# Kernel tuning notes

Hardware: AMD Instinct MI355X
Metric: run time of the kernel (lower is better)

Reference implementation:

```python
import jax, jax.numpy as jnp
import numpy as np

N_NODES = 100000
N_EDGES = 1600000
D_FEAT = 64
K = 8
AVG_DEGREE = 16


def setup_inputs() -> dict:
    key = jax.random.key(0)
    k1, k2, k3, k4 = jax.random.split(key, 4)
    x = jax.random.normal(k1, (N_NODES, D_FEAT), dtype=jnp.float32)
    # scale weights ~1/degree so repeated propagation stays bounded
    edge_weight = jax.random.uniform(k2, (N_EDGES,), dtype=jnp.float32) / AVG_DEGREE
    src = jax.random.randint(k3, (N_EDGES,), 0, N_NODES)
    dst = jax.random.randint(k4, (N_EDGES,), 0, N_NODES)
    return {"x": x, "edge_weight": edge_weight, "src": src, "dst": dst}


def reference(x, edge_weight, src, dst):
    # Prop.forward: x = spmm(adj, x) repeated K times; returned value is adj^K @ x.
    # (The in-place y.add_(x) accumulator mutates the input tensor but is not returned.)
    n = x.shape[0]
    w = edge_weight[:, None]  # [E,1]

    def step(h, _):
        # one spmm: out[dst] += w * h[src]
        h = jax.ops.segment_sum(w * h[src], dst, num_segments=n)
        return h, None

    x, _ = jax.lax.scan(step, x, None, length=K)
    return x
```

## Files before the change

### kernel.cpp

```cpp
#include <hip/hip_runtime.h>

#define N_NODES 100000
#define N_EDGES 1600000
#define D_FEAT  64
#define K_STEPS 8
#define NB_SCAN ((N_NODES + 255) / 256)

typedef unsigned long long u64;
typedef float f4 __attribute__((ext_vector_type(4)));

__global__ void k_zero(int* __restrict__ p, int n) {
    int i = blockIdx.x * blockDim.x + threadIdx.x;
    if (i < n) p[i] = 0;
}

__global__ void k_hist(const int* __restrict__ dst, int* __restrict__ counts,
                       int* __restrict__ rank, int n) {
    int i = blockIdx.x * blockDim.x + threadIdx.x;
    if (i < n) rank[i] = atomicAdd(&counts[dst[i]], 1);
}

__global__ void k_bsum(const int* __restrict__ counts, int* __restrict__ blockSums, int n) {
    __shared__ int ws[4];
    int t = threadIdx.x;
    int i = blockIdx.x * 256 + t;
    int c = (i < n) ? counts[i] : 0;
    for (int off = 32; off; off >>= 1) c += __shfl_down(c, off);
    if ((t & 63) == 0) ws[t >> 6] = c;
    __syncthreads();
    if (t == 0) blockSums[blockIdx.x] = ws[0] + ws[1] + ws[2] + ws[3];
}

__global__ void k_sscan(const int* __restrict__ blockSums, int* __restrict__ blockPrefix,
                        int* __restrict__ offsets, int nb, int n) {
    __shared__ int sh[512];
    int t = threadIdx.x;
    int v = (t < nb) ? blockSums[t] : 0;
    sh[t] = v;
    __syncthreads();
    for (int off = 1; off < 512; off <<= 1) {
        int u = (t >= off) ? sh[t - off] : 0;
        __syncthreads();
        sh[t] += u;
        __syncthreads();
    }
    if (t < nb) blockPrefix[t] = sh[t] - v;
    if (t == 511) offsets[n] = sh[511];
}

__global__ void k_bscan(const int* __restrict__ counts, const int* __restrict__ blockPrefix,
                        int* __restrict__ offsets, int n) {
    __shared__ int sh[256];
    int t = threadIdx.x;
    int i = blockIdx.x * 256 + t;
    int c = (i < n) ? counts[i] : 0;
    sh[t] = c;
    __syncthreads();
    for (int off = 1; off < 256; off <<= 1) {
        int u = (t >= off) ? sh[t - off] : 0;
        __syncthreads();
        sh[t] += u;
        __syncthreads();
    }
    int excl = sh[t] - c + blockPrefix[blockIdx.x];
    if (i < n) offsets[i] = excl;
}

__global__ void k_scatter(const int* __restrict__ src, const int* __restrict__ dst,
                          const float* __restrict__ w, const int* __restrict__ offsets,
                          const int* __restrict__ rank, u64* __restrict__ csr, int n) {
    int i = blockIdx.x * blockDim.x + threadIdx.x;
    if (i < n) {
        int d = dst[i];
        int pos = offsets[d] + rank[i];
        u64 p = ((u64)__float_as_uint(w[i]) << 32) | (unsigned)src[i];
        __builtin_nontemporal_store(p, &csr[pos]);
    }
}

__global__ void k_prop(const float* __restrict__ hin, float* __restrict__ hout,
                       const int* __restrict__ offsets,
                       const u64* __restrict__ csr, int n) {
    int wave = (blockIdx.x * blockDim.x + threadIdx.x) >> 6;
    int lane = threadIdx.x & 63;
    if (wave >= n) return;
    int b = offsets[wave];
    int e = offsets[wave + 1];
    int eg = lane >> 3;
    int fl = lane & 7;
    f4 a0 = {0.f, 0.f, 0.f, 0.f};
    f4 a1 = {0.f, 0.f, 0.f, 0.f};
    for (int i = b + eg; i < e; i += 8) {
        u64 p   = __builtin_nontemporal_load(&csr[i]);
        int s   = (int)(p & 0xffffffffu);
        float w = __uint_as_float((unsigned)(p >> 32));
        const f4* row = reinterpret_cast<const f4*>(&hin[((size_t)s << 6) + (fl << 3)]);
        f4 v0 = row[0];
        f4 v1 = row[1];
        a0.x = fmaf(w, v0.x, a0.x);
        a0.y = fmaf(w, v0.y, a0.y);
        a0.z = fmaf(w, v0.z, a0.z);
        a0.w = fmaf(w, v0.w, a0.w);
        a1.x = fmaf(w, v1.x, a1.x);
        a1.y = fmaf(w, v1.y, a1.y);
        a1.z = fmaf(w, v1.z, a1.z);
        a1.w = fmaf(w, v1.w, a1.w);
    }
    #pragma unroll
    for (int off = 8; off < 64; off <<= 1) {
        a0.x += __shfl_xor(a0.x, off);
        a0.y += __shfl_xor(a0.y, off);
        a0.z += __shfl_xor(a0.z, off);
        a0.w += __shfl_xor(a0.w, off);
        a1.x += __shfl_xor(a1.x, off);
        a1.y += __shfl_xor(a1.y, off);
        a1.z += __shfl_xor(a1.z, off);
        a1.w += __shfl_xor(a1.w, off);
    }
    if (eg == 0) {
        f4* o = reinterpret_cast<f4*>(&hout[((size_t)wave << 6) + (fl << 3)]);
        __builtin_nontemporal_store(a0, &o[0]);
        __builtin_nontemporal_store(a1, &o[1]);
    }
}

extern "C" void kernel_launch(void* const* d_in, const int* in_sizes, int n_in,
                              void* d_out, int out_size, void* d_ws, size_t ws_size,
                              hipStream_t stream) {
    const float* x   = (const float*)d_in[0];
    const float* ew  = (const float*)d_in[1];
    const int*   src = (const int*)d_in[2];
    const int*   dst = (const int*)d_in[3];
    float* out = (float*)d_out;

    float* hA         = (float*)d_ws;
    int*   rank       = (int*)d_ws;
    u64*   csr        = (u64*)(hA + (size_t)N_NODES * D_FEAT);
    int*   offsets    = (int*)(csr + N_EDGES);
    int*   counts     = offsets + (N_NODES + 1);
    int*   blockSums  = counts + N_NODES;
    int*   blockPref  = blockSums + NB_SCAN;

    k_zero<<<(N_NODES + 255) / 256, 256, 0, stream>>>(counts, N_NODES);
    k_hist<<<(N_EDGES + 255) / 256, 256, 0, stream>>>(dst, counts, rank, N_EDGES);
    k_bsum<<<NB_SCAN, 256, 0, stream>>>(counts, blockSums, N_NODES);
    k_sscan<<<1, 512, 0, stream>>>(blockSums, blockPref, offsets, NB_SCAN, N_NODES);
    k_bscan<<<NB_SCAN, 256, 0, stream>>>(counts, blockPref, offsets, N_NODES);
    k_scatter<<<(N_EDGES + 255) / 256, 256, 0, stream>>>(src, dst, ew, offsets, rank,
                                                         csr, N_EDGES);

    const int prop_grid = (N_NODES * 64 + 255) / 256;
    const float* in = x;
    for (int k = 0; k < K_STEPS; ++k) {
        float* o = ((k & 1) == 0) ? hA : out;
        k_prop<<<prop_grid, 256, 0, stream>>>(in, o, offsets, csr, N_NODES);
        in = o;
    }
}
```

Baseline: 615.8 us.

## Sort CSR edges within each destination by source tile, use cached output stores

The CSR build now groups each destination's edges by source-index tile (16 tiles). It does this with a per-tile histogram, a per-node tile prefix scan, and tile-aware scatter positions. The aim is more locality and coherence in the gathers of hin rows during propagation. The output stores in k_prop also switch from nontemporal to normal stores, so the next step's reads may hit in cache. In exchange, preprocessing gets larger: a 16x counts array, an extra kernel, and more atomic spread.

```diff
diff --git a/kernel.cpp b/kernel.cpp
--- a/kernel.cpp
+++ b/kernel.cpp
@@ -5,19 +5,40 @@
 #define D_FEAT  64
 #define K_STEPS 8
 #define NB_SCAN ((N_NODES + 255) / 256)
+#define TILES   16
+#define TILE_W  6250
 
 typedef unsigned long long u64;
 typedef float f4 __attribute__((ext_vector_type(4)));
+
+__device__ __forceinline__ int src_tile(int s) { return (int)((unsigned)s / (unsigned)TILE_W); }
 
 __global__ void k_zero(int* __restrict__ p, int n) {
     int i = blockIdx.x * blockDim.x + threadIdx.x;
     if (i < n) p[i] = 0;
 }
 
-__global__ void k_hist(const int* __restrict__ dst, int* __restrict__ counts,
-                       int* __restrict__ rank, int n) {
+__global__ void k_hist(const int* __restrict__ dst, const int* __restrict__ src,
+                       int* __restrict__ cnt16, int* __restrict__ rank, int n) {
     int i = blockIdx.x * blockDim.x + threadIdx.x;
-    if (i < n) rank[i] = atomicAdd(&counts[dst[i]], 1);
+    if (i < n) {
+        int t = src_tile(src[i]);
+        rank[i] = atomicAdd(&cnt16[t * N_NODES + dst[i]], 1);
+    }
+}
+
+__global__ void k_tilescan(const int* __restrict__ cnt16, int* __restrict__ tilePre,
+                           int* __restrict__ counts, int n) {
+    int v = blockIdx.x * blockDim.x + threadIdx.x;
+    if (v >= n) return;
+    int run = 0;
+    #pragma unroll
+    for (int t = 0; t < TILES; ++t) {
+        int c = cnt16[t * N_NODES + v];
+        tilePre[t * N_NODES + v] = run;
+        run += c;
+    }
+    counts[v] = run;
 }
 
 __global__ void k_bsum(const int* __restrict__ counts, int* __restrict__ blockSums, int n) {
@@ -68,12 +89,15 @@
 
 __global__ void k_scatter(const int* __restrict__ src, const int* __restrict__ dst,
                           const float* __restrict__ w, const int* __restrict__ offsets,
-                          const int* __restrict__ rank, u64* __restrict__ csr, int n) {
+                          const int* __restrict__ tilePre, const int* __restrict__ rank,
+                          u64* __restrict__ csr, int n) {
     int i = blockIdx.x * blockDim.x + threadIdx.x;
     if (i < n) {
+        int s = src[i];
         int d = dst[i];
-        int pos = offsets[d] + rank[i];
-        u64 p = ((u64)__float_as_uint(w[i]) << 32) | (unsigned)src[i];
+        int t = src_tile(s);
+        int pos = offsets[d] + tilePre[t * N_NODES + d] + rank[i];
+        u64 p = ((u64)__float_as_uint(w[i]) << 32) | (unsigned)s;
         __builtin_nontemporal_store(p, &csr[pos]);
     }
 }
@@ -119,8 +143,8 @@
     }
     if (eg == 0) {
         f4* o = reinterpret_cast<f4*>(&hout[((size_t)wave << 6) + (fl << 3)]);
-        __builtin_nontemporal_store(a0, &o[0]);
-        __builtin_nontemporal_store(a1, &o[1]);
+        o[0] = a0;
+        o[1] = a1;
     }
 }
 
@@ -135,19 +159,22 @@
 
     float* hA         = (float*)d_ws;
     int*   rank       = (int*)d_ws;
+    int*   cnt16      = rank + N_EDGES;
+    int*   tilePre    = cnt16 + TILES * N_NODES;
     u64*   csr        = (u64*)(hA + (size_t)N_NODES * D_FEAT);
     int*   offsets    = (int*)(csr + N_EDGES);
     int*   counts     = offsets + (N_NODES + 1);
     int*   blockSums  = counts + N_NODES;
     int*   blockPref  = blockSums + NB_SCAN;
 
-    k_zero<<<(N_NODES + 255) / 256, 256, 0, stream>>>(counts, N_NODES);
-    k_hist<<<(N_EDGES + 255) / 256, 256, 0, stream>>>(dst, counts, rank, N_EDGES);
+    k_zero<<<(TILES * N_NODES + 255) / 256, 256, 0, stream>>>(cnt16, TILES * N_NODES);
+    k_hist<<<(N_EDGES + 255) / 256, 256, 0, stream>>>(dst, src, cnt16, rank, N_EDGES);
+    k_tilescan<<<(N_NODES + 255) / 256, 256, 0, stream>>>(cnt16, tilePre, counts, N_NODES);
     k_bsum<<<NB_SCAN, 256, 0, stream>>>(counts, blockSums, N_NODES);
     k_sscan<<<1, 512, 0, stream>>>(blockSums, blockPref, offsets, NB_SCAN, N_NODES);
     k_bscan<<<NB_SCAN, 256, 0, stream>>>(counts, blockPref, offsets, N_NODES);
-    k_scatter<<<(N_EDGES + 255) / 256, 256, 0, stream>>>(src, dst, ew, offsets, rank,
-                                                         csr, N_EDGES);
+    k_scatter<<<(N_EDGES + 255) / 256, 256, 0, stream>>>(src, dst, ew, offsets, tilePre,
+                                                         rank, csr, N_EDGES);
 
     const int prop_grid = (N_NODES * 64 + 255) / 256;
     const float* in = x;
```

After: 612.4 us. No clear change (-0.6%).

## Split features into eight sliced layouts and propagate per slice

Applied to the files above, without the earlier changes.

Reshapes the node feature matrix into eight 8-feature slices, each stored contiguously, so every propagation block gathers one slice. One wave now handles one node for a single slice, with one scalar FMA per lane. Added reshape and unshape kernels convert the layout before and after the eight steps. The intent is a smaller gather working set per slice, but block indexing interleaves slices, so all slices are still touched concurrently. It also re-reads each node's CSR edge list once per slice, eight times per step, and launches eight times as many waves with less work each.

```diff
diff --git a/kernel.cpp b/kernel.cpp
--- a/kernel.cpp
+++ b/kernel.cpp
@@ -5,9 +5,11 @@
 #define D_FEAT  64
 #define K_STEPS 8
 #define NB_SCAN ((N_NODES + 255) / 256)
+#define SLICE_F 8
+#define SLICES  8
+#define SLICE_ELEMS ((size_t)N_NODES * SLICE_F)
 
 typedef unsigned long long u64;
-typedef float f4 __attribute__((ext_vector_type(4)));
 
 __global__ void k_zero(int* __restrict__ p, int n) {
     int i = blockIdx.x * blockDim.x + threadIdx.x;
@@ -78,50 +80,47 @@
     }
 }
 
-__global__ void k_prop(const float* __restrict__ hin, float* __restrict__ hout,
-                       const int* __restrict__ offsets,
-                       const u64* __restrict__ csr, int n) {
-    int wave = (blockIdx.x * blockDim.x + threadIdx.x) >> 6;
-    int lane = threadIdx.x & 63;
-    if (wave >= n) return;
-    int b = offsets[wave];
-    int e = offsets[wave + 1];
+__global__ void k_reshape(const float* __restrict__ x, float* __restrict__ hsl, int total) {
+    int tid = blockIdx.x * blockDim.x + threadIdx.x;
+    if (tid >= total) return;
+    int f = tid & 7;
+    int v = (tid >> 3) % N_NODES;
+    int s = tid / (N_NODES * 8);
+    hsl[tid] = x[(size_t)v * D_FEAT + s * 8 + f];
+}
+
+__global__ void k_unshape(const float* __restrict__ hsl, float* __restrict__ out, int total) {
+    int tid = blockIdx.x * blockDim.x + threadIdx.x;
+    if (tid >= total) return;
+    int j = tid & 63;
+    int v = tid >> 6;
+    out[tid] = hsl[(size_t)(j >> 3) * SLICE_ELEMS + (size_t)v * SLICE_F + (j & 7)];
+}
+
+__global__ __launch_bounds__(256)
+void k_prop_slice(const float* __restrict__ hin, float* __restrict__ hout,
+                  const int* __restrict__ offsets, const u64* __restrict__ csr, int n) {
+    int slice = blockIdx.x & 7;
+    int node  = (blockIdx.x >> 3) * 4 + (threadIdx.x >> 6);
+    int lane  = threadIdx.x & 63;
+    if (node >= n) return;
+    int b = offsets[node];
+    int e = offsets[node + 1];
     int eg = lane >> 3;
     int fl = lane & 7;
-    f4 a0 = {0.f, 0.f, 0.f, 0.f};
-    f4 a1 = {0.f, 0.f, 0.f, 0.f};
+    const float* hs = hin + (size_t)slice * SLICE_ELEMS;
+    float acc = 0.f;
     for (int i = b + eg; i < e; i += 8) {
         u64 p   = __builtin_nontemporal_load(&csr[i]);
         int s   = (int)(p & 0xffffffffu);
         float w = __uint_as_float((unsigned)(p >> 32));
-        const f4* row = reinterpret_cast<const f4*>(&hin[((size_t)s << 6) + (fl << 3)]);
-        f4 v0 = row[0];
-        f4 v1 = row[1];
-        a0.x = fmaf(w, v0.x, a0.x);
-        a0.y = fmaf(w, v0.y, a0.y);
-        a0.z = fmaf(w, v0.z, a0.z);
-        a0.w = fmaf(w, v0.w, a0.w);
-        a1.x = fmaf(w, v1.x, a1.x);
-        a1.y = fmaf(w, v1.y, a1.y);
-        a1.z = fmaf(w, v1.z, a1.z);
-        a1.w = fmaf(w, v1.w, a1.w);
+        acc = fmaf(w, hs[s * SLICE_F + fl], acc);
     }
-    #pragma unroll
-    for (int off = 8; off < 64; off <<= 1) {
-        a0.x += __shfl_xor(a0.x, off);
-        a0.y += __shfl_xor(a0.y, off);
-        a0.z += __shfl_xor(a0.z, off);
-        a0.w += __shfl_xor(a0.w, off);
-        a1.x += __shfl_xor(a1.x, off);
-        a1.y += __shfl_xor(a1.y, off);
-        a1.z += __shfl_xor(a1.z, off);
-        a1.w += __shfl_xor(a1.w, off);
-    }
-    if (eg == 0) {
-        f4* o = reinterpret_cast<f4*>(&hout[((size_t)wave << 6) + (fl << 3)]);
-        __builtin_nontemporal_store(a0, &o[0]);
-        __builtin_nontemporal_store(a1, &o[1]);
-    }
+    acc += __shfl_xor(acc, 8);
+    acc += __shfl_xor(acc, 16);
+    acc += __shfl_xor(acc, 32);
+    if (eg == 0)
+        hout[(size_t)slice * SLICE_ELEMS + (size_t)node * SLICE_F + fl] = acc;
 }
 
 extern "C" void kernel_launch(void* const* d_in, const int* in_sizes, int n_in,
@@ -133,13 +132,15 @@
     const int*   dst = (const int*)d_in[3];
     float* out = (float*)d_out;
 
-    float* hA         = (float*)d_ws;
+    float* hS0        = (float*)d_ws;
     int*   rank       = (int*)d_ws;
-    u64*   csr        = (u64*)(hA + (size_t)N_NODES * D_FEAT);
+    u64*   csr        = (u64*)(hS0 + (size_t)N_NODES * D_FEAT);
     int*   offsets    = (int*)(csr + N_EDGES);
     int*   counts     = offsets + (N_NODES + 1);
     int*   blockSums  = counts + N_NODES;
     int*   blockPref  = blockSums + NB_SCAN;
+
+    float* hS1 = (float*)d_out;
 
     k_zero<<<(N_NODES + 255) / 256, 256, 0, stream>>>(counts, N_NODES);
     k_hist<<<(N_EDGES + 255) / 256, 256, 0, stream>>>(dst, counts, rank, N_EDGES);
@@ -149,11 +150,14 @@
     k_scatter<<<(N_EDGES + 255) / 256, 256, 0, stream>>>(src, dst, ew, offsets, rank,
                                                          csr, N_EDGES);
 
-    const int prop_grid = (N_NODES * 64 + 255) / 256;
-    const float* in = x;
+    const int total = N_NODES * D_FEAT;
+    k_reshape<<<(total + 255) / 256, 256, 0, stream>>>(x, hS0, total);
+
+    const int prop_grid = SLICES * ((N_NODES + 3) / 4);
     for (int k = 0; k < K_STEPS; ++k) {
-        float* o = ((k & 1) == 0) ? hA : out;
-        k_prop<<<prop_grid, 256, 0, stream>>>(in, o, offsets, csr, N_NODES);
-        in = o;
+        const float* in = ((k & 1) == 0) ? hS0 : hS1;
+        float*       o  = ((k & 1) == 0) ? hS1 : hS0;
+        k_prop_slice<<<prop_grid, 256, 0, stream>>>(in, o, offsets, csr, N_NODES);
     }
+    k_unshape<<<(total + 255) / 256, 256, 0, stream>>>(hS0, out, total);
 }
```

Measured after the change: 2.396 ms. 289% more time.
